# Kernel tuning notes

Measured on AMD Instinct MI355X. Metric: run time of the kernel, lower is better.

The kernel has to match this reference:

```python
import jax, jax.numpy as jnp
import numpy as np

EPS = 1e-05


def setup_inputs() -> dict:
    key = jax.random.key(0)
    ks = jax.random.split(key, 7)
    T, d = 8192, 512
    h = jax.random.normal(ks[0], (T, d), dtype=jnp.float32)
    ln_w = jax.random.normal(ks[1], (d,), dtype=jnp.float32) * 0.1
    ln_b = jax.random.normal(ks[2], (d,), dtype=jnp.float32) * 0.1
    w_q = jax.random.normal(ks[3], (d, d), dtype=jnp.float32) * 0.1
    w_k = jax.random.normal(ks[4], (d, d), dtype=jnp.float32) * 0.1
    w_v = jax.random.normal(ks[5], (d, d), dtype=jnp.float32) * 0.1
    w_o = jax.random.normal(ks[6], (d, d), dtype=jnp.float32) * 0.1
    return {"h": h, "ln_w": ln_w, "ln_b": ln_b,
            "w_q": w_q, "w_k": w_k, "w_v": w_v, "w_o": w_o}


def reference(h, ln_w, ln_b, w_q, w_k, w_v, w_o):
    T, d = h.shape
    # LayerNorm (biased variance, matching torch)
    mu = jnp.mean(h, axis=-1, keepdims=True)
    var = jnp.mean(jnp.square(h - mu), axis=-1, keepdims=True)
    h_norm = (h - mu) * jax.lax.rsqrt(var + EPS) * ln_w + ln_b
    # nn.Linear applies x @ W.T
    q = h_norm @ w_q.T  # [T, d]
    k = h_norm @ w_k.T
    v = h_norm @ w_v.T
    scores = (q @ k.T) * (1.0 / jnp.sqrt(jnp.float32(d)))  # [T, T]
    causal = jnp.tril(jnp.ones((T, T), dtype=bool))
    scores = jnp.where(causal, scores, -jnp.inf)
    attn = jax.nn.softmax(scores, axis=-1)
    out = (attn @ v) @ w_o.T
    return h + out
```

## Files before the change

### kernel.cpp

```cpp
#include <hip/hip_runtime.h>
#include <stdint.h>

#define T_SEQ 8192
#define DMODEL 512

typedef __attribute__((ext_vector_type(8))) short bfx8;
typedef __attribute__((ext_vector_type(4))) float fx4;

__device__ __forceinline__ unsigned short f2bf(float f) {
    uint32_t u = __float_as_uint(f);
    u += 0x7fffu + ((u >> 16) & 1u);
    return (unsigned short)(u >> 16);
}
__device__ __forceinline__ float bf2f(unsigned short s) {
    return __uint_as_float(((uint32_t)s) << 16);
}

__device__ __forceinline__ void gload16(const void* g, void* l) {
    __builtin_amdgcn_global_load_lds(
        (const __attribute__((address_space(1))) unsigned int*)g,
        (__attribute__((address_space(3))) unsigned int*)l,
        16, 0, 0);
}

__device__ __forceinline__ void fence_barrier() {
    asm volatile("" ::: "memory");
    __builtin_amdgcn_s_barrier();
    asm volatile("" ::: "memory");
}

__global__ __launch_bounds__(256) void cvt_bf16_kernel(const float* __restrict__ src,
                                                       unsigned short* __restrict__ dst, int n) {
    int i = (blockIdx.x * 256 + threadIdx.x) * 8;
    if (i >= n) return;
    fx4 a = *(const fx4*)(src + i);
    fx4 b = *(const fx4*)(src + i + 4);
    bfx8 o;
    o[0] = f2bf(a[0]); o[1] = f2bf(a[1]); o[2] = f2bf(a[2]); o[3] = f2bf(a[3]);
    o[4] = f2bf(b[0]); o[5] = f2bf(b[1]); o[6] = f2bf(b[2]); o[7] = f2bf(b[3]);
    *(bfx8*)(dst + i) = o;
}

__global__ __launch_bounds__(256) void layernorm_kernel(const float* __restrict__ h,
                                                        const float* __restrict__ w,
                                                        const float* __restrict__ b,
                                                        unsigned short* __restrict__ out) {
    int wv = threadIdx.x >> 6, lane = threadIdx.x & 63;
    int row = blockIdx.x * 4 + wv;
    const float* hr = h + (size_t)row * DMODEL + lane * 8;
    fx4 x0 = *(const fx4*)hr;
    fx4 x1 = *(const fx4*)(hr + 4);
    float s  = x0[0]+x0[1]+x0[2]+x0[3]+x1[0]+x1[1]+x1[2]+x1[3];
    float ss = x0[0]*x0[0]+x0[1]*x0[1]+x0[2]*x0[2]+x0[3]*x0[3]
             + x1[0]*x1[0]+x1[1]*x1[1]+x1[2]*x1[2]+x1[3]*x1[3];
    #pragma unroll
    for (int m = 1; m < 64; m <<= 1) { s += __shfl_xor(s, m); ss += __shfl_xor(ss, m); }
    float mu  = s * (1.0f / DMODEL);
    float var = ss * (1.0f / DMODEL) - mu * mu;
    float r = rsqrtf(var + 1e-5f);
    const float* wp = w + lane * 8; const float* bp = b + lane * 8;
    fx4 w0 = *(const fx4*)wp, w1 = *(const fx4*)(wp + 4);
    fx4 b0 = *(const fx4*)bp, b1 = *(const fx4*)(bp + 4);
    bfx8 o;
    o[0] = f2bf((x0[0]-mu)*r*w0[0] + b0[0]);
    o[1] = f2bf((x0[1]-mu)*r*w0[1] + b0[1]);
    o[2] = f2bf((x0[2]-mu)*r*w0[2] + b0[2]);
    o[3] = f2bf((x0[3]-mu)*r*w0[3] + b0[3]);
    o[4] = f2bf((x1[0]-mu)*r*w1[0] + b1[0]);
    o[5] = f2bf((x1[1]-mu)*r*w1[1] + b1[1]);
    o[6] = f2bf((x1[2]-mu)*r*w1[2] + b1[2]);
    o[7] = f2bf((x1[3]-mu)*r*w1[3] + b1[3]);
    *(bfx8*)(out + (size_t)row * DMODEL + lane * 8) = o;
}

template<int RESID>
__global__ __launch_bounds__(256, 2) void gemm_bt_kernel(
    const unsigned short* __restrict__ A,
    const unsigned short* __restrict__ B,
    unsigned short* __restrict__ Cb,
    float* __restrict__ Cf,
    const float* __restrict__ resid,
    int M, int N, int K)
{
    __shared__ unsigned short At[128 * 64];
    __shared__ unsigned short Bt[128 * 64];
    int tid = threadIdx.x;
    int wv = tid >> 6, lane = tid & 63, l15 = lane & 15, l4 = lane >> 4;
    int wr = wv >> 1, wc = wv & 1;
    int row0 = blockIdx.y * 128;
    int col0 = blockIdx.x * 128;
    fx4 acc[4][4] = {};
    const char* Abase = (const char*)(A + (size_t)row0 * K);
    const char* Bbase = (const char*)(B + (size_t)col0 * K);
    for (int kt = 0; kt < K; kt += 64) {
        #pragma unroll
        for (int ch = 0; ch < 4; ch++) {
            int bix = (ch * 256 + tid) * 16;
            int r = bix >> 7;
            int sb = (bix & 127) ^ ((r & 7) << 4);
            bfx8 va = *(const bfx8*)(Abase + (size_t)r * (K * 2) + kt * 2 + sb);
            bfx8 vb = *(const bfx8*)(Bbase + (size_t)r * (K * 2) + kt * 2 + sb);
            *(bfx8*)((char*)At + bix) = va;
            *(bfx8*)((char*)Bt + bix) = vb;
        }
        __syncthreads();
        #pragma unroll
        for (int ks = 0; ks < 2; ks++) {
            bfx8 af[4], bf[4];
            #pragma unroll
            for (int m = 0; m < 4; m++) {
                int ra = wr * 64 + m * 16 + l15;
                int ka = (ks * 64 + l4 * 16) ^ ((ra & 7) << 4);
                af[m] = *(const bfx8*)((const char*)At + ra * 128 + ka);
                int rb = wc * 64 + m * 16 + l15;
                int kb = (ks * 64 + l4 * 16) ^ ((rb & 7) << 4);
                bf[m] = *(const bfx8*)((const char*)Bt + rb * 128 + kb);
            }
            #pragma unroll
            for (int m = 0; m < 4; m++)
                #pragma unroll
                for (int n = 0; n < 4; n++)
                    acc[m][n] = __builtin_amdgcn_mfma_f32_16x16x32_bf16(af[m], bf[n], acc[m][n], 0, 0, 0);
        }
        __syncthreads();
    }
    #pragma unroll
    for (int m = 0; m < 4; m++)
        #pragma unroll
        for (int n = 0; n < 4; n++)
            #pragma unroll
            for (int r = 0; r < 4; r++) {
                int row = row0 + wr * 64 + m * 16 + l4 * 4 + r;
                int col = col0 + wc * 64 + n * 16 + l15;
                float v = acc[m][n][r];
                size_t o = (size_t)row * N + col;
                if (RESID) Cf[o] = v + resid[o];
                else       Cb[o] = f2bf(v);
            }
}

__global__ __launch_bounds__(256) void transpose_kernel(const unsigned short* __restrict__ v,
                                                        unsigned short* __restrict__ vt) {
    __shared__ unsigned short tile[64][80];
    int t = threadIdx.x;
    int r0 = blockIdx.x * 64;
    int c0 = blockIdx.y * 64;
    int r = t >> 2, cw = (t & 3) * 16;
    const unsigned short* src = v + (size_t)(r0 + r) * DMODEL + c0 + cw;
    bfx8 a = *(const bfx8*)src;
    bfx8 b = *(const bfx8*)(src + 8);
    #pragma unroll
    for (int j = 0; j < 8; j++) { tile[r][cw + j] = a[j]; tile[r][cw + 8 + j] = b[j]; }
    __syncthreads();
    int dc = t >> 2, rb = (t & 3) * 16;
    bfx8 o0, o1;
    #pragma unroll
    for (int j = 0; j < 8; j++) { o0[j] = tile[rb + j][dc]; o1[j] = tile[rb + 8 + j][dc]; }
    unsigned short* dst = vt + (size_t)(c0 + dc) * T_SEQ + r0 + rb;
    *(bfx8*)dst = o0;
    *(bfx8*)(dst + 8) = o1;
}

__global__ __launch_bounds__(512)
void flash3_kernel(
    const unsigned short* __restrict__ q,
    const unsigned short* __restrict__ k,
    const unsigned short* __restrict__ vt,
    unsigned short* __restrict__ opart,
    float* __restrict__ mbuf, float* __restrict__ lbuf,
    int CH, int NBLK)
{
    __shared__ unsigned short Q_lds[64 * 512];
    __shared__ unsigned short KV_lds[64 * 512];
    __shared__ unsigned short p_lds[64 * 64];
    __shared__ float red_lds[4][2][16];
    __shared__ float alpha_lds[64];

    int tid = threadIdx.x;
    int wv = tid >> 6, lane = tid & 63, l15 = lane & 15, l4 = lane >> 4;

    int L = blockIdx.x;
    int bid = (L & 7) * (NBLK >> 3) + (L >> 3);

    int c = 0;
    while (bid >= 128 * (c + 1) - CH * (c + 1) * c / 2) c++;
    int qi = CH * c + (bid - (128 * c - CH * c * (c - 1) / 2));
    int R0 = qi * 64;
    int kv_begin = c * CH * 64;
    int kv_end = min(kv_begin + CH * 64, R0 + 64);
    int ntile = (kv_end - kv_begin) >> 6;

    int s = wv >> 1, hh = wv & 1;
    int g = wv & 1, cc = wv >> 1;

    fx4 acc[2][8] = {};
    float m_run[4], l_half[4];
    #pragma unroll
    for (int r = 0; r < 4; r++) { m_run[r] = -INFINITY; l_half[r] = 0.f; }

    const float rscale = 0.044194173824159216f;

    auto stageQ = [&]() {
        const char* qb = (const char*)q + (size_t)R0 * 1024;
        #pragma unroll
        for (int j = 0; j < 8; j++) {
            int seg = wv * 8 + j;
            int sw = (seg & 7) << 4;
            const char* gp = qb + (size_t)seg * 1024 + ((lane * 16) ^ sw);
            gload16(gp, (char*)Q_lds + seg * 1024);
        }
    };
    auto stageK = [&](int kv0) {
        const char* kb = (const char*)k + (size_t)kv0 * 1024;
        #pragma unroll
        for (int j = 0; j < 8; j++) {
            int seg = wv * 8 + j;
            int sw = (seg & 7) << 4;
            const char* gp = kb + (size_t)seg * 1024 + ((lane * 16) ^ sw);
            gload16(gp, (char*)KV_lds + seg * 1024);
        }
    };
    auto stageV = [&](int kv0) {
        const char* vb = (const char*)vt + (size_t)kv0 * 2;
        #pragma unroll
        for (int j = 0; j < 8; j++) {
            int seg = wv * 8 + j;
            int dr = seg * 8 + (lane >> 3);
            int sw = (dr & 7) << 4;
            const char* gp = vb + (size_t)dr * (T_SEQ * 2) + (((lane & 7) * 16) ^ sw);
            gload16(gp, (char*)KV_lds + seg * 1024);
        }
    };

    stageQ();
    stageK(kv_begin);

    for (int it = 0; it < ntile; it++) {
        int kv0 = kv_begin + it * 64;

        asm volatile("s_waitcnt vmcnt(0)" ::: "memory");
        fence_barrier();
        __builtin_amdgcn_sched_barrier(0);

        fx4 sf[2] = {};
        int ra = s * 16 + l15;
        int qsw = (ra & 7) << 4;
        #pragma unroll
        for (int ks = 0; ks < 16; ks++) {
            bfx8 qa = *(const bfx8*)((const char*)Q_lds + ra * 1024 + ((ks * 64 + l4 * 16) ^ qsw));
            #pragma unroll
            for (int n = 0; n < 2; n++) {
                int krow = hh * 32 + n * 16 + l15;
                int kb2 = (ks * 64 + l4 * 16) ^ ((krow & 7) << 4);
                bfx8 bfr = *(const bfx8*)((const char*)KV_lds + krow * 1024 + kb2);
                sf[n] = __builtin_amdgcn_mfma_f32_16x16x32_bf16(qa, bfr, sf[n], 0, 0, 0);
            }
        }
        float sv[2][4];
        #pragma unroll
        for (int n = 0; n < 2; n++) {
            int col = kv0 + hh * 32 + n * 16 + l15;
            #pragma unroll
            for (int r = 0; r < 4; r++) {
                int row = R0 + s * 16 + l4 * 4 + r;
                sv[n][r] = (col > row) ? -INFINITY : sf[n][r] * rscale;
            }
        }
        #pragma unroll
        for (int r = 0; r < 4; r++) {
            float x = fmaxf(sv[0][r], sv[1][r]);
            x = fmaxf(x, __shfl_xor(x, 1));
            x = fmaxf(x, __shfl_xor(x, 2));
            x = fmaxf(x, __shfl_xor(x, 4));
            x = fmaxf(x, __shfl_xor(x, 8));
            if (l15 == 0) red_lds[s][hh][l4 * 4 + r] = x;
        }
        asm volatile("s_waitcnt lgkmcnt(0)" ::: "memory");
        fence_barrier();

        stageV(kv0);

        float al[4];
        #pragma unroll
        for (int r = 0; r < 4; r++) {
            int row = l4 * 4 + r;
            float mh = fmaxf(red_lds[s][0][row], red_lds[s][1][row]);
            float mn = fmaxf(m_run[r], mh);
            al[r] = __expf(m_run[r] - mn);
            m_run[r] = mn;
        }
        if (hh == 0 && l15 == 0) {
            #pragma unroll
            for (int r = 0; r < 4; r++) alpha_lds[s * 16 + l4 * 4 + r] = al[r];
        }
        float psum[2][4];
        #pragma unroll
        for (int n = 0; n < 2; n++)
            #pragma unroll
            for (int r = 0; r < 4; r++) {
                float p = __expf(sv[n][r] - m_run[r]);
                int prow = s * 16 + l4 * 4 + r;
                int col = hh * 32 + n * 16 + l15;
                int pb = prow * 128 + ((col * 2) ^ ((prow & 7) << 4));
                *(unsigned short*)((char*)p_lds + pb) = f2bf(p);
                psum[n][r] = p;
            }
        #pragma unroll
        for (int r = 0; r < 4; r++) {
            float x = psum[0][r] + psum[1][r];
            x += __shfl_xor(x, 1); x += __shfl_xor(x, 2);
            x += __shfl_xor(x, 4); x += __shfl_xor(x, 8);
            l_half[r] = l_half[r] * al[r] + x;
        }
        asm volatile("s_waitcnt lgkmcnt(0) vmcnt(0)" ::: "memory");
        fence_barrier();
        __builtin_amdgcn_sched_barrier(0);

        float apv[2][4];
        #pragma unroll
        for (int m = 0; m < 2; m++)
            #pragma unroll
            for (int r = 0; r < 4; r++)
                apv[m][r] = alpha_lds[g * 32 + m * 16 + l4 * 4 + r];
        #pragma unroll
        for (int m = 0; m < 2; m++)
            #pragma unroll
            for (int n = 0; n < 8; n++)
                #pragma unroll
                for (int r = 0; r < 4; r++)
                    acc[m][n][r] *= apv[m][r];
        #pragma unroll
        for (int ks = 0; ks < 2; ks++) {
            bfx8 pa[2];
            #pragma unroll
            for (int m = 0; m < 2; m++) {
                int prow = g * 32 + m * 16 + l15;
                int pb = (ks * 64 + l4 * 16) ^ ((prow & 7) << 4);
                pa[m] = *(const bfx8*)((const char*)p_lds + prow * 128 + pb);
            }
            #pragma unroll
            for (int n = 0; n < 8; n++) {
                int dr = cc * 128 + n * 16 + l15;
                int vb2 = (ks * 64 + l4 * 16) ^ ((dr & 7) << 4);
                bfx8 vfr = *(const bfx8*)((const char*)KV_lds + dr * 128 + vb2);
                acc[0][n] = __builtin_amdgcn_mfma_f32_16x16x32_bf16(pa[0], vfr, acc[0][n], 0, 0, 0);
                acc[1][n] = __builtin_amdgcn_mfma_f32_16x16x32_bf16(pa[1], vfr, acc[1][n], 0, 0, 0);
            }
        }
        asm volatile("s_waitcnt lgkmcnt(0)" ::: "memory");
        fence_barrier();

        if (it + 1 < ntile) stageK(kv0 + 64);
    }

    #pragma unroll
    for (int m = 0; m < 2; m++)
        #pragma unroll
        for (int n = 0; n < 8; n++)
            #pragma unroll
            for (int r = 0; r < 4; r++) {
                int rowl = g * 32 + m * 16 + l4 * 4 + r;
                int col = cc * 128 + n * 16 + l15;
                opart[((size_t)bid * 64 + rowl) * DMODEL + col] = f2bf(acc[m][n][r]);
            }
    if (l15 == 0) {
        #pragma unroll
        for (int r = 0; r < 4; r++) red_lds[s][hh][l4 * 4 + r] = l_half[r];
    }
    __syncthreads();
    if (hh == 0 && l15 == 0) {
        #pragma unroll
        for (int r = 0; r < 4; r++) {
            int rr = l4 * 4 + r;
            int rowl = s * 16 + rr;
            lbuf[(size_t)bid * 64 + rowl] = red_lds[s][0][rr] + red_lds[s][1][rr];
            mbuf[(size_t)bid * 64 + rowl] = m_run[r];
        }
    }
}

__global__ __launch_bounds__(256) void combine2_kernel(
    const unsigned short* __restrict__ opart,
    const float* __restrict__ mbuf, const float* __restrict__ lbuf,
    unsigned short* __restrict__ attn, int CH)
{
    int tid = threadIdx.x;
    int row = blockIdx.x * 4 + (tid >> 6);
    int col = (tid & 63) * 8;
    int qi = row >> 6, rowl = row & 63;
    int nch = qi / CH + 1;
    float M = -INFINITY;
    for (int c = 0; c < nch; c++) {
        int pidx = 128 * c - CH * c * (c - 1) / 2 + (qi - CH * c);
        M = fmaxf(M, mbuf[(size_t)pidx * 64 + rowl]);
    }
    float L = 0.f;
    float accv[8] = {0.f,0.f,0.f,0.f,0.f,0.f,0.f,0.f};
    for (int c = 0; c < nch; c++) {
        int pidx = 128 * c - CH * c * (c - 1) / 2 + (qi - CH * c);
        float e = __expf(mbuf[(size_t)pidx * 64 + rowl] - M);
        L += lbuf[(size_t)pidx * 64 + rowl] * e;
        bfx8 v = *(const bfx8*)(opart + ((size_t)pidx * 64 + rowl) * DMODEL + col);
        #pragma unroll
        for (int j = 0; j < 8; j++) accv[j] += e * bf2f((unsigned short)v[j]);
    }
    float invL = 1.0f / L;
    bfx8 o;
    #pragma unroll
    for (int j = 0; j < 8; j++) o[j] = f2bf(accv[j] * invL);
    *(bfx8*)(attn + (size_t)row * DMODEL + col) = o;
}

extern "C" void kernel_launch(void* const* d_in, const int* in_sizes, int n_in,
                              void* d_out, int out_size, void* d_ws, size_t ws_size,
                              hipStream_t stream) {
    const float* h   = (const float*)d_in[0];
    const float* lnw = (const float*)d_in[1];
    const float* lnb = (const float*)d_in[2];
    const float* wq  = (const float*)d_in[3];
    const float* wk  = (const float*)d_in[4];
    const float* wv  = (const float*)d_in[5];
    const float* wo  = (const float*)d_in[6];
    float* out = (float*)d_out;

    char* ws = (char*)d_ws;
    size_t off = 0;
    auto alloc = [&](size_t bytes) {
        char* p = ws + off;
        off += (bytes + 255) & ~(size_t)255;
        return p;
    };
    const size_t TD2 = (size_t)T_SEQ * DMODEL * 2;
    unsigned short* hn  = (unsigned short*)alloc(TD2);
    unsigned short* wqb = (unsigned short*)alloc((size_t)DMODEL * DMODEL * 2);
    unsigned short* wkb = (unsigned short*)alloc((size_t)DMODEL * DMODEL * 2);
    unsigned short* wvb = (unsigned short*)alloc((size_t)DMODEL * DMODEL * 2);
    unsigned short* wob = (unsigned short*)alloc((size_t)DMODEL * DMODEL * 2);
    unsigned short* qb  = (unsigned short*)alloc(TD2);
    unsigned short* kb  = (unsigned short*)alloc(TD2);
    unsigned short* vb  = (unsigned short*)alloc(TD2);
    unsigned short* vtb = (unsigned short*)alloc(TD2);

    int CH = 8, NBLK = 1088;
    {
        size_t need = off + 2 * ((1088u * 64 * 4 + 255) & ~(size_t)255)
                    + (((size_t)1088 * 64 * 512 * 2 + 255) & ~(size_t)255);
        if (need > ws_size) { CH = 16; NBLK = 576; }
    }
    float* mbuf = (float*)alloc((size_t)NBLK * 64 * 4);
    float* lbuf = (float*)alloc((size_t)NBLK * 64 * 4);
    unsigned short* opart = (unsigned short*)alloc((size_t)NBLK * 64 * 512 * 2);
    unsigned short* attnb = kb;

    cvt_bf16_kernel<<<dim3(128), dim3(256), 0, stream>>>(wq, wqb, DMODEL * DMODEL);
    cvt_bf16_kernel<<<dim3(128), dim3(256), 0, stream>>>(wk, wkb, DMODEL * DMODEL);
    cvt_bf16_kernel<<<dim3(128), dim3(256), 0, stream>>>(wv, wvb, DMODEL * DMODEL);
    cvt_bf16_kernel<<<dim3(128), dim3(256), 0, stream>>>(wo, wob, DMODEL * DMODEL);

    layernorm_kernel<<<dim3(T_SEQ / 4), dim3(256), 0, stream>>>(h, lnw, lnb, hn);

    dim3 ggrid(DMODEL / 128, T_SEQ / 128);
    gemm_bt_kernel<0><<<ggrid, dim3(256), 0, stream>>>(hn, wqb, qb, nullptr, nullptr, T_SEQ, DMODEL, DMODEL);
    gemm_bt_kernel<0><<<ggrid, dim3(256), 0, stream>>>(hn, wkb, kb, nullptr, nullptr, T_SEQ, DMODEL, DMODEL);
    gemm_bt_kernel<0><<<ggrid, dim3(256), 0, stream>>>(hn, wvb, vb, nullptr, nullptr, T_SEQ, DMODEL, DMODEL);

    transpose_kernel<<<dim3(T_SEQ / 64, DMODEL / 64), dim3(256), 0, stream>>>(vb, vtb);

    flash3_kernel<<<dim3(NBLK), dim3(512), 0, stream>>>(qb, kb, vtb, opart, mbuf, lbuf, CH, NBLK);

    combine2_kernel<<<dim3(T_SEQ / 4), dim3(256), 0, stream>>>(opart, mbuf, lbuf, attnb, CH);

    gemm_bt_kernel<1><<<ggrid, dim3(256), 0, stream>>>(attnb, wob, nullptr, out, h, T_SEQ, DMODEL, DMODEL);
}
```

Baseline: 312.2 us.

## Fuse QKV projections into one GEMM and load V fragments directly from global

The three Q/K/V projection GEMMs are merged into one GEMM over a concatenated weight matrix, writing an interleaved QKV buffer with row stride 1536. This removes two kernel launches and reads the normalized activations once instead of three times. In the attention kernel, V is no longer staged through LDS. Each wave loads its V^T fragments straight from global memory into registers, which frees the LDS buffer so the next K tile can be prefetched earlier, overlapping with the PV step. The trade-offs are uncoalesced, strided global reads for V (8 KB row stride in V^T) and higher register pressure.

```diff
diff --git a/kernel.cpp b/kernel.cpp
--- a/kernel.cpp
+++ b/kernel.cpp
@@ -3,6 +3,7 @@
 
 #define T_SEQ 8192
 #define DMODEL 512
+#define QKV_LD 1536
 
 typedef __attribute__((ext_vector_type(8))) short bfx8;
 typedef __attribute__((ext_vector_type(4))) float fx4;
@@ -140,13 +141,13 @@
 }
 
 __global__ __launch_bounds__(256) void transpose_kernel(const unsigned short* __restrict__ v,
-                                                        unsigned short* __restrict__ vt) {
+                                                        unsigned short* __restrict__ vt, int ld) {
     __shared__ unsigned short tile[64][80];
     int t = threadIdx.x;
     int r0 = blockIdx.x * 64;
     int c0 = blockIdx.y * 64;
     int r = t >> 2, cw = (t & 3) * 16;
-    const unsigned short* src = v + (size_t)(r0 + r) * DMODEL + c0 + cw;
+    const unsigned short* src = v + (size_t)(r0 + r) * ld + c0 + cw;
     bfx8 a = *(const bfx8*)src;
     bfx8 b = *(const bfx8*)(src + 8);
     #pragma unroll
@@ -162,7 +163,7 @@
 }
 
 __global__ __launch_bounds__(512)
-void flash3_kernel(
+void flash4_kernel(
     const unsigned short* __restrict__ q,
     const unsigned short* __restrict__ k,
     const unsigned short* __restrict__ vt,
@@ -171,7 +172,7 @@
     int CH, int NBLK)
 {
     __shared__ unsigned short Q_lds[64 * 512];
-    __shared__ unsigned short KV_lds[64 * 512];
+    __shared__ unsigned short K_lds[64 * 512];
     __shared__ unsigned short p_lds[64 * 64];
     __shared__ float red_lds[4][2][16];
     __shared__ float alpha_lds[64];
@@ -201,34 +202,23 @@
     const float rscale = 0.044194173824159216f;
 
     auto stageQ = [&]() {
-        const char* qb = (const char*)q + (size_t)R0 * 1024;
+        const char* qb = (const char*)q + (size_t)R0 * (QKV_LD * 2);
         #pragma unroll
         for (int j = 0; j < 8; j++) {
             int seg = wv * 8 + j;
             int sw = (seg & 7) << 4;
-            const char* gp = qb + (size_t)seg * 1024 + ((lane * 16) ^ sw);
+            const char* gp = qb + (size_t)seg * (QKV_LD * 2) + ((lane * 16) ^ sw);
             gload16(gp, (char*)Q_lds + seg * 1024);
         }
     };
     auto stageK = [&](int kv0) {
-        const char* kb = (const char*)k + (size_t)kv0 * 1024;
+        const char* kb = (const char*)k + (size_t)kv0 * (QKV_LD * 2);
         #pragma unroll
         for (int j = 0; j < 8; j++) {
             int seg = wv * 8 + j;
             int sw = (seg & 7) << 4;
-            const char* gp = kb + (size_t)seg * 1024 + ((lane * 16) ^ sw);
-            gload16(gp, (char*)KV_lds + seg * 1024);
-        }
-    };
-    auto stageV = [&](int kv0) {
-        const char* vb = (const char*)vt + (size_t)kv0 * 2;
-        #pragma unroll
-        for (int j = 0; j < 8; j++) {
-            int seg = wv * 8 + j;
-            int dr = seg * 8 + (lane >> 3);
-            int sw = (dr & 7) << 4;
-            const char* gp = vb + (size_t)dr * (T_SEQ * 2) + (((lane & 7) * 16) ^ sw);
-            gload16(gp, (char*)KV_lds + seg * 1024);
+            const char* gp = kb + (size_t)seg * (QKV_LD * 2) + ((lane * 16) ^ sw);
+            gload16(gp, (char*)K_lds + seg * 1024);
         }
     };
 
@@ -252,7 +242,7 @@
             for (int n = 0; n < 2; n++) {
                 int krow = hh * 32 + n * 16 + l15;
                 int kb2 = (ks * 64 + l4 * 16) ^ ((krow & 7) << 4);
-                bfx8 bfr = *(const bfx8*)((const char*)KV_lds + krow * 1024 + kb2);
+                bfx8 bfr = *(const bfx8*)((const char*)K_lds + krow * 1024 + kb2);
                 sf[n] = __builtin_amdgcn_mfma_f32_16x16x32_bf16(qa, bfr, sf[n], 0, 0, 0);
             }
         }
@@ -278,7 +268,13 @@
         asm volatile("s_waitcnt lgkmcnt(0)" ::: "memory");
         fence_barrier();
 
-        stageV(kv0);
+        if (it + 1 < ntile) stageK(kv0 + 64);
+
+        const unsigned short* vrow = vt + (size_t)(cc * 128 + l15) * T_SEQ + kv0 + l4 * 8;
+        bfx8 vf0[8];
+        #pragma unroll
+        for (int n = 0; n < 8; n++)
+            vf0[n] = *(const bfx8*)(vrow + (size_t)n * 16 * T_SEQ);
 
         float al[4];
         #pragma unroll
@@ -312,7 +308,7 @@
             x += __shfl_xor(x, 4); x += __shfl_xor(x, 8);
             l_half[r] = l_half[r] * al[r] + x;
         }
-        asm volatile("s_waitcnt lgkmcnt(0) vmcnt(0)" ::: "memory");
+        asm volatile("s_waitcnt lgkmcnt(0)" ::: "memory");
         fence_barrier();
         __builtin_amdgcn_sched_barrier(0);
 
@@ -329,28 +325,35 @@
                 #pragma unroll
                 for (int r = 0; r < 4; r++)
                     acc[m][n][r] *= apv[m][r];
-        #pragma unroll
-        for (int ks = 0; ks < 2; ks++) {
-            bfx8 pa[2];
-            #pragma unroll
-            for (int m = 0; m < 2; m++) {
-                int prow = g * 32 + m * 16 + l15;
-                int pb = (ks * 64 + l4 * 16) ^ ((prow & 7) << 4);
-                pa[m] = *(const bfx8*)((const char*)p_lds + prow * 128 + pb);
-            }
+        {
+            bfx8 pa0, pa1;
+            {
+                int prow0 = g * 32 + l15;
+                int prow1 = g * 32 + 16 + l15;
+                pa0 = *(const bfx8*)((const char*)p_lds + prow0 * 128 + ((l4 * 16) ^ ((prow0 & 7) << 4)));
+                pa1 = *(const bfx8*)((const char*)p_lds + prow1 * 128 + ((l4 * 16) ^ ((prow1 & 7) << 4)));
+            }
+            bfx8 vf1[8];
+            #pragma unroll
+            for (int n = 0; n < 8; n++)
+                vf1[n] = *(const bfx8*)(vrow + (size_t)n * 16 * T_SEQ + 32);
             #pragma unroll
             for (int n = 0; n < 8; n++) {
-                int dr = cc * 128 + n * 16 + l15;
-                int vb2 = (ks * 64 + l4 * 16) ^ ((dr & 7) << 4);
-                bfx8 vfr = *(const bfx8*)((const char*)KV_lds + dr * 128 + vb2);
-                acc[0][n] = __builtin_amdgcn_mfma_f32_16x16x32_bf16(pa[0], vfr, acc[0][n], 0, 0, 0);
-                acc[1][n] = __builtin_amdgcn_mfma_f32_16x16x32_bf16(pa[1], vfr, acc[1][n], 0, 0, 0);
-            }
-        }
-        asm volatile("s_waitcnt lgkmcnt(0)" ::: "memory");
-        fence_barrier();
-
-        if (it + 1 < ntile) stageK(kv0 + 64);
+                acc[0][n] = __builtin_amdgcn_mfma_f32_16x16x32_bf16(pa0, vf0[n], acc[0][n], 0, 0, 0);
+                acc[1][n] = __builtin_amdgcn_mfma_f32_16x16x32_bf16(pa1, vf0[n], acc[1][n], 0, 0, 0);
+            }
+            {
+                int prow0 = g * 32 + l15;
+                int prow1 = g * 32 + 16 + l15;
+                pa0 = *(const bfx8*)((const char*)p_lds + prow0 * 128 + ((64 + l4 * 16) ^ ((prow0 & 7) << 4)));
+                pa1 = *(const bfx8*)((const char*)p_lds + prow1 * 128 + ((64 + l4 * 16) ^ ((prow1 & 7) << 4)));
+            }
+            #pragma unroll
+            for (int n = 0; n < 8; n++) {
+                acc[0][n] = __builtin_amdgcn_mfma_f32_16x16x32_bf16(pa0, vf1[n], acc[0][n], 0, 0, 0);
+                acc[1][n] = __builtin_amdgcn_mfma_f32_16x16x32_bf16(pa1, vf1[n], acc[1][n], 0, 0, 0);
+            }
+        }
     }
 
     #pragma unroll
@@ -431,15 +434,13 @@
         return p;
     };
     const size_t TD2 = (size_t)T_SEQ * DMODEL * 2;
-    unsigned short* hn  = (unsigned short*)alloc(TD2);
-    unsigned short* wqb = (unsigned short*)alloc((size_t)DMODEL * DMODEL * 2);
-    unsigned short* wkb = (unsigned short*)alloc((size_t)DMODEL * DMODEL * 2);
-    unsigned short* wvb = (unsigned short*)alloc((size_t)DMODEL * DMODEL * 2);
-    unsigned short* wob = (unsigned short*)alloc((size_t)DMODEL * DMODEL * 2);
-    unsigned short* qb  = (unsigned short*)alloc(TD2);
-    unsigned short* kb  = (unsigned short*)alloc(TD2);
-    unsigned short* vb  = (unsigned short*)alloc(TD2);
-    unsigned short* vtb = (unsigned short*)alloc(TD2);
+    const size_t W2  = (size_t)DMODEL * DMODEL * 2;
+    unsigned short* hn   = (unsigned short*)alloc(TD2);
+    unsigned short* wqkv = (unsigned short*)alloc(3 * W2);
+    unsigned short* wob  = (unsigned short*)alloc(W2);
+    unsigned short* qkvb = (unsigned short*)alloc((size_t)T_SEQ * QKV_LD * 2);
+    unsigned short* vtb  = (unsigned short*)alloc(TD2);
+    unsigned short* attnb= (unsigned short*)alloc(TD2);
 
     int CH = 8, NBLK = 1088;
     {
@@ -450,25 +451,25 @@
     float* mbuf = (float*)alloc((size_t)NBLK * 64 * 4);
     float* lbuf = (float*)alloc((size_t)NBLK * 64 * 4);
     unsigned short* opart = (unsigned short*)alloc((size_t)NBLK * 64 * 512 * 2);
-    unsigned short* attnb = kb;
-
-    cvt_bf16_kernel<<<dim3(128), dim3(256), 0, stream>>>(wq, wqb, DMODEL * DMODEL);
-    cvt_bf16_kernel<<<dim3(128), dim3(256), 0, stream>>>(wk, wkb, DMODEL * DMODEL);
-    cvt_bf16_kernel<<<dim3(128), dim3(256), 0, stream>>>(wv, wvb, DMODEL * DMODEL);
+
+    cvt_bf16_kernel<<<dim3(128), dim3(256), 0, stream>>>(wq, wqkv,              DMODEL * DMODEL);
+    cvt_bf16_kernel<<<dim3(128), dim3(256), 0, stream>>>(wk, wqkv + DMODEL*DMODEL,   DMODEL * DMODEL);
+    cvt_bf16_kernel<<<dim3(128), dim3(256), 0, stream>>>(wv, wqkv + 2*DMODEL*DMODEL, DMODEL * DMODEL);
     cvt_bf16_kernel<<<dim3(128), dim3(256), 0, stream>>>(wo, wob, DMODEL * DMODEL);
 
     layernorm_kernel<<<dim3(T_SEQ / 4), dim3(256), 0, stream>>>(h, lnw, lnb, hn);
 
-    dim3 ggrid(DMODEL / 128, T_SEQ / 128);
-    gemm_bt_kernel<0><<<ggrid, dim3(256), 0, stream>>>(hn, wqb, qb, nullptr, nullptr, T_SEQ, DMODEL, DMODEL);
-    gemm_bt_kernel<0><<<ggrid, dim3(256), 0, stream>>>(hn, wkb, kb, nullptr, nullptr, T_SEQ, DMODEL, DMODEL);
-    gemm_bt_kernel<0><<<ggrid, dim3(256), 0, stream>>>(hn, wvb, vb, nullptr, nullptr, T_SEQ, DMODEL, DMODEL);
-
-    transpose_kernel<<<dim3(T_SEQ / 64, DMODEL / 64), dim3(256), 0, stream>>>(vb, vtb);
-
-    flash3_kernel<<<dim3(NBLK), dim3(512), 0, stream>>>(qb, kb, vtb, opart, mbuf, lbuf, CH, NBLK);
+    gemm_bt_kernel<0><<<dim3(QKV_LD / 128, T_SEQ / 128), dim3(256), 0, stream>>>(
+        hn, wqkv, qkvb, nullptr, nullptr, T_SEQ, QKV_LD, DMODEL);
+
+    transpose_kernel<<<dim3(T_SEQ / 64, DMODEL / 64), dim3(256), 0, stream>>>(
+        qkvb + 2 * DMODEL, vtb, QKV_LD);
+
+    flash4_kernel<<<dim3(NBLK), dim3(512), 0, stream>>>(
+        qkvb, qkvb + DMODEL, vtb, opart, mbuf, lbuf, CH, NBLK);
 
     combine2_kernel<<<dim3(T_SEQ / 4), dim3(256), 0, stream>>>(opart, mbuf, lbuf, attnb, CH);
 
-    gemm_bt_kernel<1><<<ggrid, dim3(256), 0, stream>>>(attnb, wob, nullptr, out, h, T_SEQ, DMODEL, DMODEL);
-}
+    gemm_bt_kernel<1><<<dim3(DMODEL / 128, T_SEQ / 128), dim3(256), 0, stream>>>(
+        attnb, wob, nullptr, out, h, T_SEQ, DMODEL, DMODEL);
+}
```

Measured after the change: 351.5 us. +12.6%, slower.
